# Optimization experiments

Hardware: AMD Instinct MI355X
Metric: run time of the kernel (lower is better)

The kernel has to match this reference:

```python
import jax, jax.numpy as jnp
import numpy as np

B, T, D, H = 64, 512, 1024, 1024


def setup_inputs() -> dict:
    key = jax.random.key(0)
    k1, k2, k3 = jax.random.split(key, 3)
    scale_x = 1.0 / np.sqrt(D)
    scale_h = 1.0 / np.sqrt(H)
    return {
        "x": jax.random.normal(k1, (B, T, D), dtype=jnp.float32),
        "Wx": jax.random.normal(k2, (D, H), dtype=jnp.float32) * scale_x,
        "Wh": jax.random.normal(k3, (H, H), dtype=jnp.float32) * scale_h,
        "b": jnp.zeros((H,), dtype=jnp.float32),
    }


def reference(x, Wx, Wh, b):
    # Simple RNN: h_t = tanh(x_t @ Wx + h_{t-1} @ Wh + b), h_0 = 0.
    # Precompute the input projection for all timesteps in one big GEMM.
    xp = jnp.einsum("btd,dh->bth", x, Wx) + b  # [B, T, H]

    def step(h, xp_t):
        h_new = jnp.tanh(xp_t + h @ Wh)  # [B, H]
        return h_new, h_new

    h0 = jnp.zeros((x.shape[0], Wh.shape[0]), dtype=x.dtype)
    _, hs = jax.lax.scan(step, h0, jnp.swapaxes(xp, 0, 1))  # hs: [T, B, H]
    return jnp.swapaxes(hs, 0, 1)  # [B, T, H]
```

## Files before the change

### kernel.cpp

```cpp
#include <hip/hip_runtime.h>
#include <hip/hip_bf16.h>
#include <hip/hip_fp16.h>
#include <cstddef>

#define BATCH 64
#define TT    512
#define DD    1024
#define HH    1024

typedef _Float16 f16x8 __attribute__((ext_vector_type(8)));
typedef _Float16 f16x4 __attribute__((ext_vector_type(4)));
typedef float    f32x4 __attribute__((ext_vector_type(4)));
typedef unsigned long long u64;

union H8U2 { f16x8 v; u64 u[2]; };
union H4U1 { f16x4 h; u64 u; };
union F16P { _Float16 h[2]; unsigned u; };

#define MFMA16(a, b, c) __builtin_amdgcn_mfma_f32_16x16x32_f16((a), (b), (c), 0, 0, 0)

__device__ __forceinline__ float fast_tanh(float x) {
    float ax = __builtin_fabsf(x);
    float e  = __expf(-2.0f * ax);
    float r  = (1.0f - e) * __builtin_amdgcn_rcpf(1.0f + e);
    unsigned ur = (__float_as_uint(r) & 0x7fffffffu) | (__float_as_uint(x) & 0x80000000u);
    return __uint_as_float(ur);
}

__device__ __forceinline__ unsigned tagok(u64 lo, u64 hi, unsigned tagr) {
    unsigned ta = (unsigned)(lo & 1u) | (((unsigned)(lo >> 32) & 1u) << 1);
    unsigned tb = (unsigned)(hi & 1u) | (((unsigned)(hi >> 32) & 1u) << 1);
    return (unsigned)(ta == tagr) & (unsigned)(tb == tagr);
}

__global__ __launch_bounds__(256) void convert_w(
    const float* __restrict__ W, _Float16* __restrict__ Wf,
    u64* __restrict__ hzero)
{
    if (hzero && blockIdx.x < 128)
        hzero[(size_t)blockIdx.x * 256 + threadIdx.x] = 0ull;

    int o2   = blockIdx.x * 256 + threadIdx.x;
    int idx  = o2 * 2;
    int e    = idx & 7;
    int lane = (idx >> 3) & 63;
    int G    = idx >> 9;
    int kk   = G & 31;
    int cg   = G >> 5;
    int c    = cg * 16 + (lane & 15);
    int k    = kk * 32 + ((lane >> 4) & 3) * 8 + e;

    float v0 = W[(size_t)k * 1024 + c];
    float v1 = W[(size_t)(k + 1) * 1024 + c];
    F16P p; p.h[0] = (_Float16)v0; p.h[1] = (_Float16)v1;
    ((unsigned*)Wf)[o2] = p.u;
}

__global__ __launch_bounds__(256, 1) void gemm_xp_mfma(
    const float* __restrict__ x,
    const _Float16* __restrict__ WxA,
    const float* __restrict__ bias,
    float* __restrict__ out)
{
    __shared__ char lds[2][32768];

    const int tid  = threadIdx.x;
    const int w    = tid >> 6;
    const int lane = tid & 63;
    const int l15  = lane & 15;
    const int lq   = lane >> 4;
    const int token0 = (blockIdx.x * 4 + w) * 16;

    f16x8 bfrag[32];
    {
        const float* xb = x + (size_t)(token0 + l15) * DD + lq * 8;
#pragma unroll
        for (int kk = 0; kk < 32; ++kk) {
            f32x4 lo = *(const f32x4*)(xb + kk * 32);
            f32x4 hi = *(const f32x4*)(xb + kk * 32 + 4);
            f16x8 f;
#pragma unroll
            for (int j = 0; j < 4; ++j) { f[j] = (_Float16)lo[j]; f[4 + j] = (_Float16)hi[j]; }
            bfrag[kk] = f;
        }
    }
#pragma unroll
    for (int kk = 0; kk < 32; ++kk) asm volatile("" : "+v"(bfrag[kk]));

    const size_t outb = (size_t)(token0 + l15) * HH + 4 * lq;

    {
        const int cg0 = blockIdx.x & 63;
        const f16x8* gp = (const f16x8*)WxA + (size_t)cg0 * 2048;
        f16x8 st[8];
#pragma unroll
        for (int j = 0; j < 8; ++j) st[j] = gp[tid + 256 * j];
#pragma unroll
        for (int j = 0; j < 8; ++j) *(f16x8*)(lds[0] + (tid + 256 * j) * 16) = st[j];
    }
    __syncthreads();

    for (int i = 0; i < 64; ++i) {
        const int cg = (i + blockIdx.x) & 63;

        f16x8 st[8];
        if (i + 1 < 64) {
            const int cgn = (i + 1 + blockIdx.x) & 63;
            const f16x8* gp = (const f16x8*)WxA + (size_t)cgn * 2048;
#pragma unroll
            for (int j = 0; j < 8; ++j) st[j] = gp[tid + 256 * j];
        }

        const char* lb = lds[i & 1];
        f32x4 acc0 = {0,0,0,0}, acc1 = {0,0,0,0}, acc2 = {0,0,0,0}, acc3 = {0,0,0,0};
#pragma unroll
        for (int q = 0; q < 8; ++q) {
            f16x8 a0 = *(const f16x8*)(lb + ((q*4 + 0) * 64 + lane) * 16);
            f16x8 a1 = *(const f16x8*)(lb + ((q*4 + 1) * 64 + lane) * 16);
            f16x8 a2 = *(const f16x8*)(lb + ((q*4 + 2) * 64 + lane) * 16);
            f16x8 a3 = *(const f16x8*)(lb + ((q*4 + 3) * 64 + lane) * 16);
            acc0 = MFMA16(a0, bfrag[q*4+0], acc0);
            acc1 = MFMA16(a1, bfrag[q*4+1], acc1);
            acc2 = MFMA16(a2, bfrag[q*4+2], acc2);
            acc3 = MFMA16(a3, bfrag[q*4+3], acc3);
        }
        f32x4 bv = *(const f32x4*)(bias + cg * 16 + 4 * lq);
        f32x4 r;
#pragma unroll
        for (int v = 0; v < 4; ++v)
            r[v] = ((acc0[v] + acc1[v]) + (acc2[v] + acc3[v])) + bv[v];
        *(f32x4*)(out + outb + cg * 16) = r;

        if (i + 1 < 64) {
            char* lw = lds[(i + 1) & 1];
#pragma unroll
            for (int j = 0; j < 8; ++j) *(f16x8*)(lw + (tid + 256 * j) * 16) = st[j];
        }
        __syncthreads();
    }
}

__global__ __launch_bounds__(256, 1) void rnn_persist(
    const _Float16* __restrict__ Whf,
    _Float16* __restrict__ hb0,
    _Float16* __restrict__ hb1,
    float* __restrict__ out)
{
    __shared__ char ldsraw[65536];

    const int tid  = threadIdx.x;
    const int bg   = blockIdx.x & 3;
    const int co4  = blockIdx.x >> 2;
    const int w    = tid >> 6;
    const int cg   = co4 * 4 + w;
    const int lane = tid & 63;
    const int l15  = lane & 15;
    const int lq   = lane >> 4;

    f16x8 afrag[32];
    {
        const f16x8* wp = (const f16x8*)Whf + (size_t)cg * 32 * 64 + lane;
#pragma unroll
        for (int kk = 0; kk < 32; ++kk) afrag[kk] = wp[(size_t)kk * 64];
    }
#pragma unroll
    for (int kk = 0; kk < 32; ++kk) asm volatile("" : "+v"(afrag[kk]));

    _Float16* hbuf[2] = {hb0, hb1};

    const int b = bg * 16 + l15;
    const int c = cg * 16 + 4 * lq;
    const size_t ob = (size_t)b * TT * HH + c;

    unsigned soff[8];
    const _Float16* src0[8];
    const _Float16* src1[8];
    unsigned ownm = 0u;
#pragma unroll
    for (int i = 0; i < 8; ++i) {
        int gi   = tid + 256 * i;
        int srow = gi >> 7;
        int scol = gi & 127;
        soff[i]  = ((unsigned)gi * 16u) ^ (unsigned)((srow & 7) << 4);
        src0[i]  = hb0 + (size_t)(bg * 16 + srow) * HH + scol * 8;
        src1[i]  = hb1 + (size_t)(bg * 16 + srow) * HH + scol * 8;
        if ((scol >> 3) == co4) ownm |= (1u << i);
    }

    const unsigned g16 = (unsigned)(c >> 3);
    const unsigned eb  = (unsigned)(l15 * 2048)
                       + ((g16 * 16u) ^ (unsigned)((l15 & 7) << 4))
                       + 8u * (unsigned)(lq & 1);

    f32x4 xq;
    {
        const float* xpp = out + ob;
        asm volatile("global_load_dwordx4 %0, %1, off" : "=v"(xq) : "v"(xpp));
    }

    H8U2 uu[8], uu2[8];

    for (int t = 0; t < TT; ++t) {
        if (t > 0) {
            const unsigned tagr = 1u + (unsigned)((t - 1) % 3);
            const _Float16* const* src = ((t + 1) & 1) ? src1 : src0;

            __builtin_amdgcn_sched_barrier(0);
            asm volatile("s_waitcnt vmcnt(1)" ::: "memory");
            __builtin_amdgcn_sched_barrier(0);

            while (true) {
                unsigned good = 1u;
#pragma unroll
                for (int i = 0; i < 8; ++i) {
                    unsigned ok1 = tagok(uu[i].u[0],  uu[i].u[1],  tagr);
                    unsigned ok2 = tagok(uu2[i].u[0], uu2[i].u[1], tagr);
                    if (!ok1) uu[i] = uu2[i];
                    good &= (ok1 | ok2 | ((ownm >> i) & 1u));
                }
                if (__all((int)good)) break;
                __builtin_amdgcn_s_sleep(1);
#pragma unroll
                for (int i = 0; i < 8; ++i)
                    asm volatile("global_load_dwordx4 %0, %1, off sc0 sc1"
                                 : "=v"(uu[i].v) : "v"(src[i]));
                __builtin_amdgcn_sched_barrier(0);
                asm volatile("s_waitcnt vmcnt(0)" ::: "memory");
                __builtin_amdgcn_sched_barrier(0);
            }

            char* lb = ldsraw + (t & 1) * 32768;
#pragma unroll
            for (int i = 0; i < 8; ++i)
                if (!((ownm >> i) & 1u))
                    *(f16x8*)(lb + soff[i]) = uu[i].v;
        }

        asm volatile("s_waitcnt lgkmcnt(0)\n\ts_barrier" ::: "memory");

        f32x4 acc0 = {0,0,0,0}, acc1 = {0,0,0,0}, acc2 = {0,0,0,0}, acc3 = {0,0,0,0};
        if (t > 0) {
            const char* lb = ldsraw + (t & 1) * 32768;
            const unsigned rbase = (unsigned)(l15 * 2048);
            const unsigned rswz  = (unsigned)((l15 & 7) << 4);
#pragma unroll
            for (int q = 0; q < 8; ++q) {
                f16x8 b0, b1, b2, b3;
                b0 = *(const f16x8*)(lb + ((rbase + ((q*16 + 0*4 + lq) * 16u)) ^ rswz));
                b1 = *(const f16x8*)(lb + ((rbase + ((q*16 + 1*4 + lq) * 16u)) ^ rswz));
                b2 = *(const f16x8*)(lb + ((rbase + ((q*16 + 2*4 + lq) * 16u)) ^ rswz));
                b3 = *(const f16x8*)(lb + ((rbase + ((q*16 + 3*4 + lq) * 16u)) ^ rswz));
                acc0 = MFMA16(afrag[q*4+0], b0, acc0);
                acc1 = MFMA16(afrag[q*4+1], b1, acc1);
                acc2 = MFMA16(afrag[q*4+2], b2, acc2);
                acc3 = MFMA16(afrag[q*4+3], b3, acc3);
            }
        }

        __builtin_amdgcn_sched_barrier(0);
        asm volatile("s_waitcnt vmcnt(0)" ::: "memory");
        __builtin_amdgcn_sched_barrier(0);

        const unsigned tagw = 1u + (unsigned)(t % 3);
        f32x4 hvv;
        H4U1 pk;
#pragma unroll
        for (int v = 0; v < 4; ++v) {
            float s = ((acc0[v] + acc1[v]) + (acc2[v] + acc3[v])) + xq[v];
            hvv[v] = fast_tanh(s);
            pk.h[v] = (_Float16)hvv[v];
        }
        pk.u = (pk.u & ~(1ull | (1ull << 32)))
             | (u64)(tagw & 1u) | ((u64)(tagw >> 1) << 32);

        if (t + 1 < TT)
            *(u64*)(ldsraw + ((t + 1) & 1) * 32768 + eb) = pk.u;

        {
            _Float16* q = hbuf[t & 1] + (size_t)b * HH + c;
            asm volatile("global_store_dwordx2 %0, %1, off sc0 sc1"
                         :: "v"(q), "v"(pk.u) : "memory");
        }
        if (t + 1 < TT) {
            const _Float16* const* src = (t & 1) ? src1 : src0;
#pragma unroll
            for (int i = 0; i < 8; ++i)
                asm volatile("global_load_dwordx4 %0, %1, off sc0 sc1"
                             : "=v"(uu[i].v) : "v"(src[i]));
        }
        {
            const float* op = out + ob + (size_t)t * HH;
            asm volatile("global_store_dwordx4 %0, %1, off"
                         :: "v"(op), "v"(hvv) : "memory");
        }
        if (t + 1 < TT) {
            const _Float16* const* src = (t & 1) ? src1 : src0;
#pragma unroll
            for (int i = 0; i < 8; ++i)
                asm volatile("global_load_dwordx4 %0, %1, off sc0 sc1"
                             : "=v"(uu2[i].v) : "v"(src[i]));
            const float* xpp = out + ob + (size_t)(t + 1) * HH;
            asm volatile("global_load_dwordx4 %0, %1, off" : "=v"(xq) : "v"(xpp));
        }
    }
}

extern "C" void kernel_launch(void* const* d_in, const int* in_sizes, int n_in,
                              void* d_out, int out_size, void* d_ws, size_t ws_size,
                              hipStream_t stream) {
    const float* x    = (const float*)d_in[0];
    const float* Wx   = (const float*)d_in[1];
    const float* Wh   = (const float*)d_in[2];
    const float* bias = (const float*)d_in[3];

    float* out = (float*)d_out;

    _Float16* Whf = (_Float16*)d_ws;
    _Float16* WxA = Whf + (1u << 20);
    _Float16* hb0 = WxA + (1u << 20);
    _Float16* hb1 = hb0 + BATCH * HH;

    convert_w<<<2048, 256, 0, stream>>>(Wh, Whf, (u64*)hb0);
    convert_w<<<2048, 256, 0, stream>>>(Wx, WxA, nullptr);

    gemm_xp_mfma<<<512, 256, 0, stream>>>(x, WxA, bias, out);

    rnn_persist<<<64, 256, 0, stream>>>(Whf, hb0, hb1, out);
}
```

Before: 2.014 ms.

## Process two batch groups per block to overlap polling with MFMA work

The persistent RNN kernel now launches half as many blocks, and each block handles two 16-row batch groups in alternation. While one group computes its matmul and tanh, the global polls for the other group's hidden state are already in flight, which is meant to hide cross-block synchronisation latency. The change drops the duplicate poll buffers and the skip for a block's own slice of the hidden state, so every slice is read back from global memory. Each block also does twice the serial work per step, and halving the block count cuts parallelism across CUs.

After: 2.047 ms. About the same (+1.6%).

```diff
diff --git a/kernel.cpp b/kernel.cpp
--- a/kernel.cpp
+++ b/kernel.cpp
@@ -146,16 +146,19 @@
     _Float16* __restrict__ hb1,
     float* __restrict__ out)
 {
-    __shared__ char ldsraw[65536];
+    __shared__ char ldsA[32768];
+    __shared__ char ldsB[32768];
 
     const int tid  = threadIdx.x;
-    const int bg   = blockIdx.x & 3;
-    const int co4  = blockIdx.x >> 2;
+    const int pair = blockIdx.x & 1;
+    const int co4  = blockIdx.x >> 1;
     const int w    = tid >> 6;
     const int cg   = co4 * 4 + w;
     const int lane = tid & 63;
     const int l15  = lane & 15;
     const int lq   = lane >> 4;
+    const int bgA  = pair * 2;
+    const int bgB  = pair * 2 + 1;
 
     f16x8 afrag[32];
     {
@@ -166,90 +169,89 @@
 #pragma unroll
     for (int kk = 0; kk < 32; ++kk) asm volatile("" : "+v"(afrag[kk]));
 
-    _Float16* hbuf[2] = {hb0, hb1};
-
-    const int b = bg * 16 + l15;
-    const int c = cg * 16 + 4 * lq;
-    const size_t ob = (size_t)b * TT * HH + c;
+    const int bA = bgA * 16 + l15;
+    const int bB = bgB * 16 + l15;
+    const int c  = cg * 16 + 4 * lq;
+    const size_t obA = (size_t)bA * TT * HH + c;
+    const size_t obB = (size_t)bB * TT * HH + c;
 
     unsigned soff[8];
-    const _Float16* src0[8];
-    const _Float16* src1[8];
-    unsigned ownm = 0u;
+    int rowA[8], rowB[8];
 #pragma unroll
     for (int i = 0; i < 8; ++i) {
         int gi   = tid + 256 * i;
         int srow = gi >> 7;
         int scol = gi & 127;
         soff[i]  = ((unsigned)gi * 16u) ^ (unsigned)((srow & 7) << 4);
-        src0[i]  = hb0 + (size_t)(bg * 16 + srow) * HH + scol * 8;
-        src1[i]  = hb1 + (size_t)(bg * 16 + srow) * HH + scol * 8;
-        if ((scol >> 3) == co4) ownm |= (1u << i);
-    }
-
-    const unsigned g16 = (unsigned)(c >> 3);
-    const unsigned eb  = (unsigned)(l15 * 2048)
-                       + ((g16 * 16u) ^ (unsigned)((l15 & 7) << 4))
-                       + 8u * (unsigned)(lq & 1);
-
-    f32x4 xq;
+        rowA[i]  = (bgA * 16 + srow) * HH + scol * 8;
+        rowB[i]  = (bgB * 16 + srow) * HH + scol * 8;
+    }
+
+    f32x4 xqA, xqB;
     {
-        const float* xpp = out + ob;
-        asm volatile("global_load_dwordx4 %0, %1, off" : "=v"(xq) : "v"(xpp));
-    }
-
-    H8U2 uu[8], uu2[8];
+        const float* pA = out + obA;
+        asm volatile("global_load_dwordx4 %0, %1, off" : "=v"(xqA) : "v"(pA));
+        const float* pB = out + obB;
+        asm volatile("global_load_dwordx4 %0, %1, off" : "=v"(xqB) : "v"(pB));
+    }
+
+    H8U2 uu[8];
+
+#define ISSUE_POLLS(rowarr, par)                                              \
+    {                                                                         \
+        const _Float16* _b = (par) ? hb1 : hb0;                               \
+        _Pragma("unroll")                                                     \
+        for (int _i = 0; _i < 8; ++_i) {                                      \
+            const _Float16* _p = _b + rowarr[_i];                             \
+            asm volatile("global_load_dwordx4 %0, %1, off sc0 sc1"            \
+                         : "=v"(uu[_i].v) : "v"(_p));                         \
+        }                                                                     \
+    }
+
+#define CHECK_RETRY(rowarr, par, tagr)                                        \
+    while (true) {                                                            \
+        unsigned _good = 1u;                                                  \
+        _Pragma("unroll")                                                     \
+        for (int _i = 0; _i < 8; ++_i)                                        \
+            _good &= tagok(uu[_i].u[0], uu[_i].u[1], (tagr));                 \
+        if (__all((int)_good)) break;                                         \
+        __builtin_amdgcn_s_sleep(1);                                          \
+        ISSUE_POLLS(rowarr, par);                                             \
+        __builtin_amdgcn_sched_barrier(0);                                    \
+        asm volatile("s_waitcnt vmcnt(0)" ::: "memory");                      \
+        __builtin_amdgcn_sched_barrier(0);                                    \
+    }
 
     for (int t = 0; t < TT; ++t) {
+        const unsigned tagr = 1u + (unsigned)((t + 2) % 3);
+        const unsigned tagw = 1u + (unsigned)(t % 3);
+        const int tn = (t + 1 < TT) ? (t + 1) : t;
+
+        __builtin_amdgcn_sched_barrier(0);
+        if (t > 0) { asm volatile("s_waitcnt vmcnt(3)" ::: "memory"); }
+        else       { asm volatile("s_waitcnt vmcnt(1)" ::: "memory"); }
+        __builtin_amdgcn_sched_barrier(0);
+
         if (t > 0) {
-            const unsigned tagr = 1u + (unsigned)((t - 1) % 3);
-            const _Float16* const* src = ((t + 1) & 1) ? src1 : src0;
-
-            __builtin_amdgcn_sched_barrier(0);
-            asm volatile("s_waitcnt vmcnt(1)" ::: "memory");
-            __builtin_amdgcn_sched_barrier(0);
-
-            while (true) {
-                unsigned good = 1u;
-#pragma unroll
-                for (int i = 0; i < 8; ++i) {
-                    unsigned ok1 = tagok(uu[i].u[0],  uu[i].u[1],  tagr);
-                    unsigned ok2 = tagok(uu2[i].u[0], uu2[i].u[1], tagr);
-                    if (!ok1) uu[i] = uu2[i];
-                    good &= (ok1 | ok2 | ((ownm >> i) & 1u));
-                }
-                if (__all((int)good)) break;
-                __builtin_amdgcn_s_sleep(1);
-#pragma unroll
-                for (int i = 0; i < 8; ++i)
-                    asm volatile("global_load_dwordx4 %0, %1, off sc0 sc1"
-                                 : "=v"(uu[i].v) : "v"(src[i]));
-                __builtin_amdgcn_sched_barrier(0);
-                asm volatile("s_waitcnt vmcnt(0)" ::: "memory");
-                __builtin_amdgcn_sched_barrier(0);
-            }
-
-            char* lb = ldsraw + (t & 1) * 32768;
+            CHECK_RETRY(rowA, (t + 1) & 1, tagr);
 #pragma unroll
             for (int i = 0; i < 8; ++i)
-                if (!((ownm >> i) & 1u))
-                    *(f16x8*)(lb + soff[i]) = uu[i].v;
-        }
-
+                *(f16x8*)(ldsA + soff[i]) = uu[i].v;
+        }
         asm volatile("s_waitcnt lgkmcnt(0)\n\ts_barrier" ::: "memory");
+
+        if (t > 0) ISSUE_POLLS(rowB, (t + 1) & 1);
 
         f32x4 acc0 = {0,0,0,0}, acc1 = {0,0,0,0}, acc2 = {0,0,0,0}, acc3 = {0,0,0,0};
         if (t > 0) {
-            const char* lb = ldsraw + (t & 1) * 32768;
             const unsigned rbase = (unsigned)(l15 * 2048);
             const unsigned rswz  = (unsigned)((l15 & 7) << 4);
 #pragma unroll
             for (int q = 0; q < 8; ++q) {
-                f16x8 b0, b1, b2, b3;
-                b0 = *(const f16x8*)(lb + ((rbase + ((q*16 + 0*4 + lq) * 16u)) ^ rswz));
-                b1 = *(const f16x8*)(lb + ((rbase + ((q*16 + 1*4 + lq) * 16u)) ^ rswz));
-                b2 = *(const f16x8*)(lb + ((rbase + ((q*16 + 2*4 + lq) * 16u)) ^ rswz));
-                b3 = *(const f16x8*)(lb + ((rbase + ((q*16 + 3*4 + lq) * 16u)) ^ rswz));
+                f16x8 b0 = *(const f16x8*)(ldsA + ((rbase + ((q*16 + 0*4 + lq) * 16u)) ^ rswz));
+                f16x8 b1 = *(const f16x8*)(ldsA + ((rbase + ((q*16 + 1*4 + lq) * 16u)) ^ rswz));
+                f16x8 b2 = *(const f16x8*)(ldsA + ((rbase + ((q*16 + 2*4 + lq) * 16u)) ^ rswz));
+                f16x8 b3 = *(const f16x8*)(ldsA + ((rbase + ((q*16 + 3*4 + lq) * 16u)) ^ rswz));
                 acc0 = MFMA16(afrag[q*4+0], b0, acc0);
                 acc1 = MFMA16(afrag[q*4+1], b1, acc1);
                 acc2 = MFMA16(afrag[q*4+2], b2, acc2);
@@ -257,52 +259,82 @@
             }
         }
 
-        __builtin_amdgcn_sched_barrier(0);
-        asm volatile("s_waitcnt vmcnt(0)" ::: "memory");
-        __builtin_amdgcn_sched_barrier(0);
-
-        const unsigned tagw = 1u + (unsigned)(t % 3);
-        f32x4 hvv;
-        H4U1 pk;
-#pragma unroll
-        for (int v = 0; v < 4; ++v) {
-            float s = ((acc0[v] + acc1[v]) + (acc2[v] + acc3[v])) + xq[v];
-            hvv[v] = fast_tanh(s);
-            pk.h[v] = (_Float16)hvv[v];
-        }
-        pk.u = (pk.u & ~(1ull | (1ull << 32)))
-             | (u64)(tagw & 1u) | ((u64)(tagw >> 1) << 32);
-
-        if (t + 1 < TT)
-            *(u64*)(ldsraw + ((t + 1) & 1) * 32768 + eb) = pk.u;
-
         {
-            _Float16* q = hbuf[t & 1] + (size_t)b * HH + c;
+            f32x4 hvv; H4U1 pk;
+#pragma unroll
+            for (int v = 0; v < 4; ++v) {
+                float s = ((acc0[v] + acc1[v]) + (acc2[v] + acc3[v])) + xqA[v];
+                hvv[v] = fast_tanh(s);
+                pk.h[v] = (_Float16)hvv[v];
+            }
+            pk.u = (pk.u & ~(1ull | (1ull << 32)))
+                 | (u64)(tagw & 1u) | ((u64)(tagw >> 1) << 32);
+
+            _Float16* q = ((t & 1) ? hb1 : hb0) + (size_t)bA * HH + c;
             asm volatile("global_store_dwordx2 %0, %1, off sc0 sc1"
                          :: "v"(q), "v"(pk.u) : "memory");
-        }
-        if (t + 1 < TT) {
-            const _Float16* const* src = (t & 1) ? src1 : src0;
-#pragma unroll
-            for (int i = 0; i < 8; ++i)
-                asm volatile("global_load_dwordx4 %0, %1, off sc0 sc1"
-                             : "=v"(uu[i].v) : "v"(src[i]));
-        }
-        {
-            const float* op = out + ob + (size_t)t * HH;
+            const float* op = out + obA + (size_t)t * HH;
             asm volatile("global_store_dwordx4 %0, %1, off"
                          :: "v"(op), "v"(hvv) : "memory");
-        }
-        if (t + 1 < TT) {
-            const _Float16* const* src = (t & 1) ? src1 : src0;
+            const float* xpp = out + obA + (size_t)tn * HH;
+            asm volatile("global_load_dwordx4 %0, %1, off" : "=v"(xqA) : "v"(xpp));
+        }
+
+        __builtin_amdgcn_sched_barrier(0);
+        asm volatile("s_waitcnt vmcnt(3)" ::: "memory");
+        __builtin_amdgcn_sched_barrier(0);
+
+        if (t > 0) {
+            CHECK_RETRY(rowB, (t + 1) & 1, tagr);
 #pragma unroll
             for (int i = 0; i < 8; ++i)
-                asm volatile("global_load_dwordx4 %0, %1, off sc0 sc1"
-                             : "=v"(uu2[i].v) : "v"(src[i]));
-            const float* xpp = out + ob + (size_t)(t + 1) * HH;
-            asm volatile("global_load_dwordx4 %0, %1, off" : "=v"(xq) : "v"(xpp));
-        }
-    }
+                *(f16x8*)(ldsB + soff[i]) = uu[i].v;
+        }
+        asm volatile("s_waitcnt lgkmcnt(0)\n\ts_barrier" ::: "memory");
+
+        if (t + 1 < TT) ISSUE_POLLS(rowA, t & 1);
+
+        acc0 = (f32x4){0,0,0,0}; acc1 = (f32x4){0,0,0,0};
+        acc2 = (f32x4){0,0,0,0}; acc3 = (f32x4){0,0,0,0};
+        if (t > 0) {
+            const unsigned rbase = (unsigned)(l15 * 2048);
+            const unsigned rswz  = (unsigned)((l15 & 7) << 4);
+#pragma unroll
+            for (int q = 0; q < 8; ++q) {
+                f16x8 b0 = *(const f16x8*)(ldsB + ((rbase + ((q*16 + 0*4 + lq) * 16u)) ^ rswz));
+                f16x8 b1 = *(const f16x8*)(ldsB + ((rbase + ((q*16 + 1*4 + lq) * 16u)) ^ rswz));
+                f16x8 b2 = *(const f16x8*)(ldsB + ((rbase + ((q*16 + 2*4 + lq) * 16u)) ^ rswz));
+                f16x8 b3 = *(const f16x8*)(ldsB + ((rbase + ((q*16 + 3*4 + lq) * 16u)) ^ rswz));
+                acc0 = MFMA16(afrag[q*4+0], b0, acc0);
+                acc1 = MFMA16(afrag[q*4+1], b1, acc1);
+                acc2 = MFMA16(afrag[q*4+2], b2, acc2);
+                acc3 = MFMA16(afrag[q*4+3], b3, acc3);
+            }
+        }
+
+        {
+            f32x4 hvv; H4U1 pk;
+#pragma unroll
+            for (int v = 0; v < 4; ++v) {
+                float s = ((acc0[v] + acc1[v]) + (acc2[v] + acc3[v])) + xqB[v];
+                hvv[v] = fast_tanh(s);
+                pk.h[v] = (_Float16)hvv[v];
+            }
+            pk.u = (pk.u & ~(1ull | (1ull << 32)))
+                 | (u64)(tagw & 1u) | ((u64)(tagw >> 1) << 32);
+
+            _Float16* q = ((t & 1) ? hb1 : hb0) + (size_t)bB * HH + c;
+            asm volatile("global_store_dwordx2 %0, %1, off sc0 sc1"
+                         :: "v"(q), "v"(pk.u) : "memory");
+            const float* op = out + obB + (size_t)t * HH;
+            asm volatile("global_store_dwordx4 %0, %1, off"
+                         :: "v"(op), "v"(hvv) : "memory");
+            const float* xpp = out + obB + (size_t)tn * HH;
+            asm volatile("global_load_dwordx4 %0, %1, off" : "=v"(xqB) : "v"(xpp));
+        }
+    }
+#undef ISSUE_POLLS
+#undef CHECK_RETRY
 }
 
 extern "C" void kernel_launch(void* const* d_in, const int* in_sizes, int n_in,
@@ -325,5 +357,5 @@
 
     gemm_xp_mfma<<<512, 256, 0, stream>>>(x, WxA, bias, out);
 
-    rnn_persist<<<64, 256, 0, stream>>>(Whf, hb0, hb1, out);
-}
+    rnn_persist<<<32, 256, 0, stream>>>(Whf, hb0, hb1, out);
+}
```
